# Kernel optimization log

Measured on AMD Instinct MI355X. Metric: run time of the kernel, lower is better.

The kernel has to match this reference:

```python
import jax, jax.numpy as jnp
import numpy as np

E = 8      # number of parts/experts
H = 128    # hidden width
D_IN = 3   # xyz coords
D_OUT = 1  # occupancy


def setup_inputs() -> dict:
    key = jax.random.key(0)
    ks = jax.random.split(key, 9)
    coords = jax.random.normal(ks[0], (1, 65536, D_IN), dtype=jnp.float32)
    s = 0.05
    return {
        "coords": coords,
        "W0": jax.random.normal(ks[1], (E, H, D_IN), dtype=jnp.float32) * s,
        "b0": jax.random.normal(ks[2], (E, H), dtype=jnp.float32) * s,
        "W1": jax.random.normal(ks[3], (E, H, H), dtype=jnp.float32) * s,
        "b1": jax.random.normal(ks[4], (E, H), dtype=jnp.float32) * s,
        "W2": jax.random.normal(ks[5], (E, H, H), dtype=jnp.float32) * s,
        "b2": jax.random.normal(ks[6], (E, H), dtype=jnp.float32) * s,
        "Wo": jax.random.normal(ks[7], (E, D_OUT, H), dtype=jnp.float32) * s,
        "bo": jax.random.normal(ks[8], (E, D_OUT), dtype=jnp.float32) * s,
    }


def reference(coords, W0, b0, W1, b1, W2, b2, Wo, bo):
    # Batched (grouped) MLP over experts: equivalent to vmap(functional_call)
    # over stacked per-part parameters in the torch module.
    # coords: [B, N, 3]; weights: [E, out, in]
    h = jax.nn.relu(jnp.einsum('bnd,ehd->ebnh', coords, W0) + b0[:, None, None, :])
    h = jax.nn.relu(jnp.einsum('ebnh,egh->ebng', h, W1) + b1[:, None, None, :])
    h = jax.nn.relu(jnp.einsum('ebnh,egh->ebng', h, W2) + b2[:, None, None, :])
    expert_out = jnp.einsum('ebnh,eoh->ebno', h, Wo) + bo[:, None, None, :]  # [E,B,N,1]
    max_occ = jnp.max(expert_out, axis=0)  # combine experts via max, [B,N,1]
    return max_occ
```

## Files before the change

kernel.cpp:

```cpp
#include <hip/hip_runtime.h>

#define NE 8
#define HD 128
#define NPTS 65536
#define TM 64
#define NT (NPTS / TM)
#define XPS 40

typedef __bf16 bf16x8 __attribute__((ext_vector_type(8)));
typedef __bf16 bf16x4 __attribute__((ext_vector_type(4)));
typedef float f32x4 __attribute__((ext_vector_type(4)));

__device__ __forceinline__ unsigned int f2bf(float f) {
    unsigned int u = __float_as_uint(f);
    u += 0x7FFFu + ((u >> 16) & 1u);
    return u >> 16;
}

__device__ __forceinline__ unsigned int fenc(float f) {
    unsigned int u = __float_as_uint(f);
    return ((int)u < 0) ? ~u : (u | 0x80000000u);
}
__device__ __forceinline__ float fdec(unsigned int u) {
    return __uint_as_float(((int)u < 0) ? (u & 0x7FFFFFFFu) : ~u);
}

__device__ __forceinline__ unsigned int swz(int row, int byte_in_row) {
    return (unsigned int)((row * 256 + byte_in_row) ^ ((row & 7) << 4));
}

__device__ __forceinline__ void bar_lds() {
    asm volatile("s_waitcnt lgkmcnt(0)\ns_barrier" ::: "memory");
}

__device__ __forceinline__ void loadA128(const unsigned short* __restrict__ Ag,
                                         bf16x8 (&a)[2][4], int tc, int lr, int lg) {
#pragma unroll
    for (int ca = 0; ca < 2; ++ca)
#pragma unroll
        for (int kb = 0; kb < 4; ++kb)
            a[ca][kb] = *(const bf16x8*)(Ag + (tc + ca * 16 + lr) * HD + kb * 32 + lg * 8);
}

__device__ __forceinline__ void gemm_core(const bf16x8 (&a)[2][4], const char* Bb,
                                          f32x4 (&acc)[2][4], int lr, int lg) {
#pragma unroll
    for (int kb = 0; kb < 4; ++kb) {
        bf16x8 b[4];
#pragma unroll
        for (int nb = 0; nb < 4; ++nb)
            b[nb] = *(const bf16x8*)(Bb + swz(nb * 16 + lr, kb * 64 + lg * 16));
#pragma unroll
        for (int ca = 0; ca < 2; ++ca)
#pragma unroll
            for (int nb = 0; nb < 4; ++nb)
                acc[ca][nb] = __builtin_amdgcn_mfma_f32_16x16x32_bf16(a[ca][kb], b[nb], acc[ca][nb], 0, 0, 0);
    }
}

__device__ __forceinline__ void epi_store(const f32x4 (&acc)[2][4], char* Db,
                                          const float4 (&bs)[2], int tc, int lr, int lg) {
#pragma unroll
    for (int ca = 0; ca < 2; ++ca) {
        int c0 = tc + ca * 16 + lg * 4;
#pragma unroll
        for (int nb = 0; nb < 4; ++nb) {
            int r = nb * 16 + lr;
            bf16x4 pk;
            pk[0] = (__bf16)fmaxf(acc[ca][nb][0] + bs[ca].x, 0.f);
            pk[1] = (__bf16)fmaxf(acc[ca][nb][1] + bs[ca].y, 0.f);
            pk[2] = (__bf16)fmaxf(acc[ca][nb][2] + bs[ca].z, 0.f);
            pk[3] = (__bf16)fmaxf(acc[ca][nb][3] + bs[ca].w, 0.f);
            *(bf16x4*)(Db + swz(r, c0 * 2)) = pk;
        }
    }
}

__global__ void prep_kernel(const float* __restrict__ W0,
                            const float* __restrict__ W1,
                            const float* __restrict__ W2,
                            unsigned int* __restrict__ W1b,
                            unsigned int* __restrict__ W2b,
                            unsigned int* __restrict__ W0p,
                            unsigned int* __restrict__ outenc) {
    int i = blockIdx.x * 256 + threadIdx.x;
    float2 v = *(const float2*)(W1 + 2 * i);
    W1b[i] = f2bf(v.x) | (f2bf(v.y) << 16);
    float2 u = *(const float2*)(W2 + 2 * i);
    W2b[i] = f2bf(u.x) | (f2bf(u.y) << 16);
    outenc[i] = 0u;
    if (i < NE * HD * 16) {
        int row = i >> 4;
        int kk = (i & 15) * 2;
        float a = (kk < 3) ? W0[row * 3 + kk] : 0.f;
        float b = (kk + 1 < 3) ? W0[row * 3 + kk + 1] : 0.f;
        W0p[i] = f2bf(a) | (f2bf(b) << 16);
    }
}

__global__ void decode_kernel(unsigned int* __restrict__ outenc) {
    int i = blockIdx.x * 256 + threadIdx.x;
    outenc[i] = __float_as_uint(fdec(outenc[i]));
}

__global__ __launch_bounds__(256, 4) void moe_expert(
    const float* __restrict__ coords,
    const float* __restrict__ b0, const float* __restrict__ b1,
    const float* __restrict__ b2,
    const float* __restrict__ Wo, const float* __restrict__ bo,
    const unsigned short* __restrict__ W0p,
    const unsigned short* __restrict__ W1b,
    const unsigned short* __restrict__ W2b,
    unsigned int* __restrict__ outenc) {
    __shared__ __align__(16) unsigned short hA[TM * HD];
    __shared__ __align__(16) unsigned short hB[TM * HD];
    __shared__ __align__(16) unsigned short Xp[TM * XPS];
    __shared__ __align__(16) float part[4 * TM];

    const int tid = threadIdx.x;
    const int lane = tid & 63;
    const int w = tid >> 6;
    const int lr = lane & 15;
    const int lg = lane >> 4;
    const int tc = w * 32;
    const int tile = blockIdx.x & (NT - 1);
    const int e = blockIdx.x >> 10;
    const int row0 = tile * TM;

    bf16x8 a0[2], a1[2][4];
#pragma unroll
    for (int ca = 0; ca < 2; ++ca)
        a0[ca] = *(const bf16x8*)(W0p + e * HD * 32 + (tc + ca * 16 + lr) * 32 + lg * 8);
    loadA128(W1b + e * HD * HD, a1, tc, lr, lg);

    if (tid < TM) {
        unsigned int* rowp = (unsigned int*)(Xp + tid * XPS);
        float c0 = coords[(row0 + tid) * 3 + 0];
        float c1 = coords[(row0 + tid) * 3 + 1];
        float c2 = coords[(row0 + tid) * 3 + 2];
        rowp[0] = f2bf(c0) | (f2bf(c1) << 16);
        rowp[1] = f2bf(c2);
#pragma unroll
        for (int i = 2; i < XPS / 2; ++i) rowp[i] = 0;
    }
    bar_lds();

    {
        bf16x8 xb[4];
#pragma unroll
        for (int nb = 0; nb < 4; ++nb)
            xb[nb] = *(const bf16x8*)(Xp + (nb * 16 + lr) * XPS + lg * 8);
        float4 bs0[2];
#pragma unroll
        for (int ca = 0; ca < 2; ++ca) bs0[ca] = *(const float4*)(b0 + e * HD + tc + ca * 16 + lg * 4);
        f32x4 acc[2][4];
#pragma unroll
        for (int ca = 0; ca < 2; ++ca)
#pragma unroll
            for (int nb = 0; nb < 4; ++nb) {
                acc[ca][nb] = (f32x4){0.f, 0.f, 0.f, 0.f};
                acc[ca][nb] = __builtin_amdgcn_mfma_f32_16x16x32_bf16(a0[ca], xb[nb], acc[ca][nb], 0, 0, 0);
            }
        epi_store(acc, (char*)hA, bs0, tc, lr, lg);
    }
    bar_lds();

    bf16x8 a2[2][4];
    loadA128(W2b + e * HD * HD, a2, tc, lr, lg);
    {
        float4 bs1[2];
#pragma unroll
        for (int ca = 0; ca < 2; ++ca) bs1[ca] = *(const float4*)(b1 + e * HD + tc + ca * 16 + lg * 4);
        f32x4 acc[2][4];
#pragma unroll
        for (int ca = 0; ca < 2; ++ca)
#pragma unroll
            for (int nb = 0; nb < 4; ++nb) acc[ca][nb] = (f32x4){0.f, 0.f, 0.f, 0.f};
        gemm_core(a1, (const char*)hA, acc, lr, lg);
        epi_store(acc, (char*)hB, bs1, tc, lr, lg);
    }
    bar_lds();

    {
        float4 bs2[2], wo[2];
#pragma unroll
        for (int ca = 0; ca < 2; ++ca) {
            int c0 = tc + ca * 16 + lg * 4;
            bs2[ca] = *(const float4*)(b2 + e * HD + c0);
            wo[ca] = *(const float4*)(Wo + e * HD + c0);
        }
        f32x4 acc[2][4];
#pragma unroll
        for (int ca = 0; ca < 2; ++ca)
#pragma unroll
            for (int nb = 0; nb < 4; ++nb) acc[ca][nb] = (f32x4){0.f, 0.f, 0.f, 0.f};
        gemm_core(a2, (const char*)hB, acc, lr, lg);

        float s[4] = {0.f, 0.f, 0.f, 0.f};
#pragma unroll
        for (int ca = 0; ca < 2; ++ca)
#pragma unroll
            for (int nb = 0; nb < 4; ++nb) {
                float v0 = fmaxf(acc[ca][nb][0] + bs2[ca].x, 0.f);
                float v1 = fmaxf(acc[ca][nb][1] + bs2[ca].y, 0.f);
                float v2 = fmaxf(acc[ca][nb][2] + bs2[ca].z, 0.f);
                float v3 = fmaxf(acc[ca][nb][3] + bs2[ca].w, 0.f);
                s[nb] += v0 * wo[ca].x + v1 * wo[ca].y + v2 * wo[ca].z + v3 * wo[ca].w;
            }
#pragma unroll
        for (int nb = 0; nb < 4; ++nb) {
            s[nb] += __shfl_xor(s[nb], 16);
            s[nb] += __shfl_xor(s[nb], 32);
        }
        if (lg == 0) {
#pragma unroll
            for (int nb = 0; nb < 4; ++nb) part[w * TM + nb * 16 + lr] = s[nb];
        }
    }
    bar_lds();

    if (tid < TM) {
        float v = part[tid] + part[TM + tid] + part[2 * TM + tid] + part[3 * TM + tid] + bo[e];
        atomicMax(&outenc[row0 + tid], fenc(v));
    }
}

extern "C" void kernel_launch(void* const* d_in, const int* in_sizes, int n_in,
                              void* d_out, int out_size, void* d_ws, size_t ws_size,
                              hipStream_t stream) {
    const float* coords = (const float*)d_in[0];
    const float* W0 = (const float*)d_in[1];
    const float* b0 = (const float*)d_in[2];
    const float* W1 = (const float*)d_in[3];
    const float* b1 = (const float*)d_in[4];
    const float* W2 = (const float*)d_in[5];
    const float* b2 = (const float*)d_in[6];
    const float* Wo = (const float*)d_in[7];
    const float* bo = (const float*)d_in[8];
    unsigned int* outenc = (unsigned int*)d_out;

    char* ws = (char*)d_ws;
    unsigned short* W1b = (unsigned short*)(ws);
    unsigned short* W2b = (unsigned short*)(ws + 262144);
    unsigned short* W0p = (unsigned short*)(ws + 524288);

    prep_kernel<<<dim3(256), dim3(256), 0, stream>>>(
        W0, W1, W2, (unsigned int*)W1b, (unsigned int*)W2b, (unsigned int*)W0p, outenc);

    moe_expert<<<dim3(NT * NE), dim3(256), 0, stream>>>(
        coords, b0, b1, b2, Wo, bo, W0p, W1b, W2b, outenc);

    decode_kernel<<<dim3(NPTS / 256), dim3(256), 0, stream>>>(outenc);
}
```

Baseline: 85.27 us.

## Stream weight fragments per k-step and reuse one LDS buffer to raise occupancy

Weight A-fragments are now loaded from global memory per k-block inside the GEMM instead of being preloaded into registers, and the separate hB and Xp LDS buffers are dropped. Layer 2 writes back into hA after an extra barrier, and layer-0 inputs are built directly in registers from coords. Launch bounds go from 4 to 8 waves per SIMD to let more blocks run at once. The trade-off is weight loads sitting on the critical path inside the MFMA loop, plus an extra barrier, which higher occupancy is meant to hide.

```diff
diff --git a/kernel.cpp b/kernel.cpp
--- a/kernel.cpp
+++ b/kernel.cpp
@@ -5,7 +5,6 @@
 #define NPTS 65536
 #define TM 64
 #define NT (NPTS / TM)
-#define XPS 40
 
 typedef __bf16 bf16x8 __attribute__((ext_vector_type(8)));
 typedef __bf16 bf16x4 __attribute__((ext_vector_type(4)));
@@ -33,20 +32,16 @@
     asm volatile("s_waitcnt lgkmcnt(0)\ns_barrier" ::: "memory");
 }
 
-__device__ __forceinline__ void loadA128(const unsigned short* __restrict__ Ag,
-                                         bf16x8 (&a)[2][4], int tc, int lr, int lg) {
-#pragma unroll
-    for (int ca = 0; ca < 2; ++ca)
-#pragma unroll
-        for (int kb = 0; kb < 4; ++kb)
-            a[ca][kb] = *(const bf16x8*)(Ag + (tc + ca * 16 + lr) * HD + kb * 32 + lg * 8);
-}
-
-__device__ __forceinline__ void gemm_core(const bf16x8 (&a)[2][4], const char* Bb,
-                                          f32x4 (&acc)[2][4], int lr, int lg) {
+__device__ __forceinline__ void gemm_stream(const unsigned short* __restrict__ Ag,
+                                            const unsigned short* Bs,
+                                            f32x4 (&acc)[2][4], int tc, int lr, int lg) {
+    const char* Bb = (const char*)Bs;
 #pragma unroll
     for (int kb = 0; kb < 4; ++kb) {
-        bf16x8 b[4];
+        bf16x8 a[2], b[4];
+#pragma unroll
+        for (int ca = 0; ca < 2; ++ca)
+            a[ca] = *(const bf16x8*)(Ag + (tc + ca * 16 + lr) * HD + kb * 32 + lg * 8);
 #pragma unroll
         for (int nb = 0; nb < 4; ++nb)
             b[nb] = *(const bf16x8*)(Bb + swz(nb * 16 + lr, kb * 64 + lg * 16));
@@ -54,23 +49,25 @@
         for (int ca = 0; ca < 2; ++ca)
 #pragma unroll
             for (int nb = 0; nb < 4; ++nb)
-                acc[ca][nb] = __builtin_amdgcn_mfma_f32_16x16x32_bf16(a[ca][kb], b[nb], acc[ca][nb], 0, 0, 0);
+                acc[ca][nb] = __builtin_amdgcn_mfma_f32_16x16x32_bf16(a[ca], b[nb], acc[ca][nb], 0, 0, 0);
     }
 }
 
 __device__ __forceinline__ void epi_store(const f32x4 (&acc)[2][4], char* Db,
-                                          const float4 (&bs)[2], int tc, int lr, int lg) {
+                                          const float* __restrict__ bias,
+                                          int tc, int lr, int lg) {
 #pragma unroll
     for (int ca = 0; ca < 2; ++ca) {
         int c0 = tc + ca * 16 + lg * 4;
+        float4 bs = *(const float4*)(bias + c0);
 #pragma unroll
         for (int nb = 0; nb < 4; ++nb) {
             int r = nb * 16 + lr;
             bf16x4 pk;
-            pk[0] = (__bf16)fmaxf(acc[ca][nb][0] + bs[ca].x, 0.f);
-            pk[1] = (__bf16)fmaxf(acc[ca][nb][1] + bs[ca].y, 0.f);
-            pk[2] = (__bf16)fmaxf(acc[ca][nb][2] + bs[ca].z, 0.f);
-            pk[3] = (__bf16)fmaxf(acc[ca][nb][3] + bs[ca].w, 0.f);
+            pk[0] = (__bf16)fmaxf(acc[ca][nb][0] + bs.x, 0.f);
+            pk[1] = (__bf16)fmaxf(acc[ca][nb][1] + bs.y, 0.f);
+            pk[2] = (__bf16)fmaxf(acc[ca][nb][2] + bs.z, 0.f);
+            pk[3] = (__bf16)fmaxf(acc[ca][nb][3] + bs.w, 0.f);
             *(bf16x4*)(Db + swz(r, c0 * 2)) = pk;
         }
     }
@@ -103,7 +100,7 @@
     outenc[i] = __float_as_uint(fdec(outenc[i]));
 }
 
-__global__ __launch_bounds__(256, 4) void moe_expert(
+__global__ __launch_bounds__(256, 8) void moe_expert(
     const float* __restrict__ coords,
     const float* __restrict__ b0, const float* __restrict__ b1,
     const float* __restrict__ b2,
@@ -113,8 +110,6 @@
     const unsigned short* __restrict__ W2b,
     unsigned int* __restrict__ outenc) {
     __shared__ __align__(16) unsigned short hA[TM * HD];
-    __shared__ __align__(16) unsigned short hB[TM * HD];
-    __shared__ __align__(16) unsigned short Xp[TM * XPS];
     __shared__ __align__(16) float part[4 * TM];
 
     const int tid = threadIdx.x;
@@ -127,32 +122,23 @@
     const int e = blockIdx.x >> 10;
     const int row0 = tile * TM;
 
-    bf16x8 a0[2], a1[2][4];
-#pragma unroll
-    for (int ca = 0; ca < 2; ++ca)
-        a0[ca] = *(const bf16x8*)(W0p + e * HD * 32 + (tc + ca * 16 + lr) * 32 + lg * 8);
-    loadA128(W1b + e * HD * HD, a1, tc, lr, lg);
-
-    if (tid < TM) {
-        unsigned int* rowp = (unsigned int*)(Xp + tid * XPS);
-        float c0 = coords[(row0 + tid) * 3 + 0];
-        float c1 = coords[(row0 + tid) * 3 + 1];
-        float c2 = coords[(row0 + tid) * 3 + 2];
-        rowp[0] = f2bf(c0) | (f2bf(c1) << 16);
-        rowp[1] = f2bf(c2);
-#pragma unroll
-        for (int i = 2; i < XPS / 2; ++i) rowp[i] = 0;
-    }
-    bar_lds();
-
     {
         bf16x8 xb[4];
 #pragma unroll
-        for (int nb = 0; nb < 4; ++nb)
-            xb[nb] = *(const bf16x8*)(Xp + (nb * 16 + lr) * XPS + lg * 8);
-        float4 bs0[2];
-#pragma unroll
-        for (int ca = 0; ca < 2; ++ca) bs0[ca] = *(const float4*)(b0 + e * HD + tc + ca * 16 + lg * 4);
+        for (int nb = 0; nb < 4; ++nb) {
+            int p = row0 + nb * 16 + lr;
+            float x = coords[p * 3 + 0];
+            float y = coords[p * 3 + 1];
+            float z = coords[p * 3 + 2];
+            bf16x8 v = {};
+            v[0] = (__bf16)x; v[1] = (__bf16)y; v[2] = (__bf16)z;
+            bf16x8 zero = {};
+            xb[nb] = (lg == 0) ? v : zero;
+        }
+        bf16x8 a0[2];
+#pragma unroll
+        for (int ca = 0; ca < 2; ++ca)
+            a0[ca] = *(const bf16x8*)(W0p + e * HD * 32 + (tc + ca * 16 + lr) * 32 + lg * 8);
         f32x4 acc[2][4];
 #pragma unroll
         for (int ca = 0; ca < 2; ++ca)
@@ -161,27 +147,30 @@
                 acc[ca][nb] = (f32x4){0.f, 0.f, 0.f, 0.f};
                 acc[ca][nb] = __builtin_amdgcn_mfma_f32_16x16x32_bf16(a0[ca], xb[nb], acc[ca][nb], 0, 0, 0);
             }
-        epi_store(acc, (char*)hA, bs0, tc, lr, lg);
+        epi_store(acc, (char*)hA, b0 + e * HD, tc, lr, lg);
     }
     bar_lds();
 
-    bf16x8 a2[2][4];
-    loadA128(W2b + e * HD * HD, a2, tc, lr, lg);
     {
-        float4 bs1[2];
-#pragma unroll
-        for (int ca = 0; ca < 2; ++ca) bs1[ca] = *(const float4*)(b1 + e * HD + tc + ca * 16 + lg * 4);
         f32x4 acc[2][4];
 #pragma unroll
         for (int ca = 0; ca < 2; ++ca)
 #pragma unroll
             for (int nb = 0; nb < 4; ++nb) acc[ca][nb] = (f32x4){0.f, 0.f, 0.f, 0.f};
-        gemm_core(a1, (const char*)hA, acc, lr, lg);
-        epi_store(acc, (char*)hB, bs1, tc, lr, lg);
+        gemm_stream(W1b + e * HD * HD, hA, acc, tc, lr, lg);
+        bar_lds();
+        epi_store(acc, (char*)hA, b1 + e * HD, tc, lr, lg);
     }
     bar_lds();
 
     {
+        f32x4 acc[2][4];
+#pragma unroll
+        for (int ca = 0; ca < 2; ++ca)
+#pragma unroll
+            for (int nb = 0; nb < 4; ++nb) acc[ca][nb] = (f32x4){0.f, 0.f, 0.f, 0.f};
+        gemm_stream(W2b + e * HD * HD, hA, acc, tc, lr, lg);
+
         float4 bs2[2], wo[2];
 #pragma unroll
         for (int ca = 0; ca < 2; ++ca) {
@@ -189,13 +178,6 @@
             bs2[ca] = *(const float4*)(b2 + e * HD + c0);
             wo[ca] = *(const float4*)(Wo + e * HD + c0);
         }
-        f32x4 acc[2][4];
-#pragma unroll
-        for (int ca = 0; ca < 2; ++ca)
-#pragma unroll
-            for (int nb = 0; nb < 4; ++nb) acc[ca][nb] = (f32x4){0.f, 0.f, 0.f, 0.f};
-        gemm_core(a2, (const char*)hB, acc, lr, lg);
-
         float s[4] = {0.f, 0.f, 0.f, 0.f};
 #pragma unroll
         for (int ca = 0; ca < 2; ++ca)
```

Measured after the change: 125.9 us. 47.6% more time.
